# Kernel optimization log

Hardware: AMD Instinct MI355X
Metric: run time of the kernel (lower is better)

Reference implementation:

```python
import jax, jax.numpy as jnp
import numpy as np
import math

K_DIM = 1024
HEADS = 16

def setup_inputs() -> dict:
    key = jax.random.key(0)
    ks = jax.random.split(key, 6)
    b, N, k = 4, 2048, K_DIM
    sc = 1.0 / math.sqrt(k)
    return {
        "x": jax.random.normal(ks[0], (b, N, k), dtype=jnp.float32),
        "Wk": jax.random.normal(ks[1], (k, k), dtype=jnp.float32) * sc,
        "Wq": jax.random.normal(ks[2], (k, k), dtype=jnp.float32) * sc,
        "Wv": jax.random.normal(ks[3], (k, k), dtype=jnp.float32) * sc,
        "Wu": jax.random.normal(ks[4], (k, k), dtype=jnp.float32) * sc,
        "bu": jax.random.normal(ks[5], (k,), dtype=jnp.float32) * 0.01,
    }

def reference(x, Wk, Wq, Wv, Wu, bu):
    b, N, k = x.shape
    h = HEADS
    s = k // h
    # torch Linear: y = x @ W^T
    Q = (x @ Wq.T).reshape(b, N, h, s).transpose(0, 2, 1, 3)  # [b,h,N,s]
    Kh = (x @ Wk.T).reshape(b, N, h, s).transpose(0, 2, 1, 3)
    V = (x @ Wv.T).reshape(b, N, h, s).transpose(0, 2, 1, 3)
    scores = jnp.einsum('bhid,bhjd->bhij', Q, Kh) / math.sqrt(s)  # [b,h,N,N]
    attn = jax.nn.softmax(scores, axis=-1)
    out = jnp.einsum('bhij,bhjd->bhid', attn, V)  # [b,h,N,s]
    out = out.transpose(0, 2, 1, 3).reshape(b, N, k)
    return out @ Wu.T + bu
```

## Files before the change

### kernel.cpp

```cpp
#include <hip/hip_runtime.h>

typedef __bf16 bf16;
typedef __bf16 bf16x4 __attribute__((ext_vector_type(4)));
typedef __bf16 bf16x8 __attribute__((ext_vector_type(8)));
typedef float  f32x4  __attribute__((ext_vector_type(4)));

#define MFMA16(a, b, c) __builtin_amdgcn_mfma_f32_16x16x32_bf16((a), (b), (c), 0, 0, 0)

__device__ __forceinline__ void async_copy16(const void* g, void* l) {
  __builtin_amdgcn_global_load_lds(
      (const __attribute__((address_space(1))) unsigned int*)g,
      (__attribute__((address_space(3))) unsigned int*)l, 16, 0, 0);
}

struct CvtArgs {
  const float* src[5];
  bf16* dst[5];
  int blk_start[6];
};
__global__ void k_cvt_all(CvtArgs a) {
  int b = blockIdx.x;
  int seg = 0;
#pragma unroll
  for (int s = 1; s < 5; ++s) seg += (b >= a.blk_start[s]);
  int i = (b - a.blk_start[seg]) * 2048 + threadIdx.x * 8;
  float4 v0 = *(const float4*)(a.src[seg] + i);
  float4 v1 = *(const float4*)(a.src[seg] + i + 4);
  bf16x8 o = { (bf16)v0.x, (bf16)v0.y, (bf16)v0.z, (bf16)v0.w,
               (bf16)v1.x, (bf16)v1.y, (bf16)v1.z, (bf16)v1.w };
  *(bf16x8*)(a.dst[seg] + i) = o;
}

template <int OUTF32>
__device__ __forceinline__ void gemm128_body(
    const bf16* __restrict__ A, const bf16* __restrict__ B, void* __restrict__ Cp,
    const float* __restrict__ bias, int m0, int n0, int N, int K) {
  __shared__ alignas(16) bf16 As[2][128 * 32];
  __shared__ alignas(16) bf16 Bs[2][128 * 32];
  const int tid = threadIdx.x;
  const int lane = tid & 63;
  const int w = tid >> 6;
  const int quad = lane >> 4;
  const int l16 = lane & 15;
  const int wr = (w >> 1) * 64;
  const int wc = (w & 1) * 64;

  const int srow = tid >> 2;
  const int skk = (tid & 3) * 8;
  const bf16* Ag = A + (long)(m0 + srow) * K + skk;
  const bf16* Bg = B + (long)(n0 + srow) * K + skk;
  const long half = 64L * K;
  bf16* AsW0 = As[0] + w * 512;
  bf16* BsW0 = Bs[0] + w * 512;
  bf16* AsW1 = As[1] + w * 512;
  bf16* BsW1 = Bs[1] + w * 512;

  f32x4 acc[4][4];
#pragma unroll
  for (int i = 0; i < 4; ++i)
#pragma unroll
    for (int j = 0; j < 4; ++j) acc[i][j] = (f32x4){0.f, 0.f, 0.f, 0.f};

  for (int k0 = 0; k0 < K; k0 += 64) {
    async_copy16(Ag + k0, AsW0);
    async_copy16(Ag + half + k0, AsW0 + 2048);
    async_copy16(Bg + k0, BsW0);
    async_copy16(Bg + half + k0, BsW0 + 2048);
    async_copy16(Ag + k0 + 32, AsW1);
    async_copy16(Ag + half + k0 + 32, AsW1 + 2048);
    async_copy16(Bg + k0 + 32, BsW1);
    async_copy16(Bg + half + k0 + 32, BsW1 + 2048);
    __syncthreads();
#pragma unroll
    for (int p = 0; p < 2; ++p) {
      const bf16* AsP = As[p];
      const bf16* BsP = Bs[p];
      bf16x8 af[4], bfr[4];
#pragma unroll
      for (int i = 0; i < 4; ++i)
        af[i] = *(const bf16x8*)&AsP[(wr + i * 16 + l16) * 32 + quad * 8];
#pragma unroll
      for (int j = 0; j < 4; ++j)
        bfr[j] = *(const bf16x8*)&BsP[(wc + j * 16 + l16) * 32 + quad * 8];
#pragma unroll
      for (int i = 0; i < 4; ++i)
#pragma unroll
        for (int j = 0; j < 4; ++j) acc[i][j] = MFMA16(af[i], bfr[j], acc[i][j]);
    }
    __syncthreads();
  }

#pragma unroll
  for (int i = 0; i < 4; ++i)
#pragma unroll
    for (int j = 0; j < 4; ++j)
#pragma unroll
      for (int r = 0; r < 4; ++r) {
        long row = m0 + wr + i * 16 + quad * 4 + r;
        int col = n0 + wc + j * 16 + l16;
        if (OUTF32)
          ((float*)Cp)[row * N + col] = acc[i][j][r] + bias[col];
        else
          ((bf16*)Cp)[row * N + col] = (bf16)acc[i][j][r];
      }
}

__global__ __launch_bounds__(256, 4) void k_gemm_qkv(
    const bf16* __restrict__ xb, const bf16* __restrict__ Wqk, bf16* __restrict__ QKb,
    const bf16* __restrict__ Wvb, bf16* __restrict__ VtG) {
  int bid = blockIdx.x;
  const bf16 *A, *B;
  bf16* C;
  int m0, n0, N;
  if (bid < 1024) {
    A = xb; B = Wqk; C = QKb;
    m0 = (bid & 63) * 128; n0 = (bid >> 6) * 128; N = 2048;
  } else {
    int id = bid - 1024;
    A = Wvb; B = xb; C = VtG;
    m0 = (id >> 6) * 128; n0 = (id & 63) * 128; N = 8192;
  }
  gemm128_body<0>(A, B, C, nullptr, m0, n0, N, 1024);
}

__global__ __launch_bounds__(256, 4) void k_gemm_out(
    const bf16* __restrict__ Ab, const bf16* __restrict__ Wub, float* __restrict__ out,
    const float* __restrict__ bu) {
  gemm128_body<1>(Ab, Wub, out, bu, blockIdx.x * 128, blockIdx.y * 128, 1024, 1024);
}

__global__ __launch_bounds__(256, 2) void k_attn(
    const bf16* __restrict__ Q, const bf16* __restrict__ Kb,
    const bf16* __restrict__ Vt, bf16* __restrict__ O) {
  __shared__ alignas(16) bf16 Ps[256][72];
  __shared__ alignas(16) bf16 Ks[64][72];
  __shared__ alignas(16) bf16 Vs[64][72];

  const int tid = threadIdx.x;
  const int lane = tid & 63;
  const int w = tid >> 6;
  const int quad = lane >> 4;
  const int l16 = lane & 15;
  const int bh = blockIdx.x;
  const int qt = blockIdx.y;
  const int bb = bh >> 4;
  const int h = bh & 15;
  const int hoff = h * 64;
  const long rowQ0 = (long)bb * 2048 + qt * 256;
  const long kv0 = (long)bb * 2048;

  {
    const bf16* p = Q + (rowQ0 + tid) * 2048 + hoff;
#pragma unroll
    for (int u = 0; u < 8; ++u) {
      bf16x8 v = *(const bf16x8*)(p + u * 8);
      bf16x8 o;
#pragma unroll
      for (int j = 0; j < 8; ++j) o[j] = (bf16)((float)v[j] * 0.125f);
      *(bf16x8*)&Ps[tid][u * 8] = o;
    }
  }
  bf16x8 bq[4][2];
#pragma unroll
  for (int g = 0; g < 4; ++g)
#pragma unroll
    for (int ss = 0; ss < 2; ++ss)
      bq[g][ss] = *(const bf16x8*)&Ps[w * 64 + g * 16 + l16][ss * 32 + quad * 8];

  f32x4 accO[4][4];
  float lp[4] = {0.f, 0.f, 0.f, 0.f};
#pragma unroll
  for (int g = 0; g < 4; ++g)
#pragma unroll
    for (int t = 0; t < 4; ++t) accO[g][t] = (f32x4){0.f, 0.f, 0.f, 0.f};

  const int srow = tid >> 2;
  const int scol = (tid & 3) * 8;
  const int c0p = ((scol & 8) << 1) | ((scol & 16) >> 2);
  const bf16* kp = Kb + (kv0 + srow) * 2048 + hoff + scol;
  const bf16* vp = Vt + (long)(hoff + srow) * 8192 + kv0 + scol;

  bf16x8 kr0 = *(const bf16x8*)kp;
  bf16x8 kr1 = *(const bf16x8*)(kp + 32);
  bf16x8 vr0 = *(const bf16x8*)vp;
  bf16x8 vr1 = *(const bf16x8*)(vp + 32);

  for (int kt = 0; kt < 32; ++kt) {
    __syncthreads();
    *(bf16x8*)&Ks[srow][scol] = kr0;
    *(bf16x8*)&Ks[srow][scol + 32] = kr1;
    {
      bf16x4 lo0 = {vr0[0], vr0[1], vr0[2], vr0[3]};
      bf16x4 hi0 = {vr0[4], vr0[5], vr0[6], vr0[7]};
      bf16x4 lo1 = {vr1[0], vr1[1], vr1[2], vr1[3]};
      bf16x4 hi1 = {vr1[4], vr1[5], vr1[6], vr1[7]};
      *(bf16x4*)&Vs[srow][c0p] = lo0;
      *(bf16x4*)&Vs[srow][c0p + 8] = hi0;
      *(bf16x4*)&Vs[srow][c0p + 32] = lo1;
      *(bf16x4*)&Vs[srow][c0p + 40] = hi1;
    }
    __syncthreads();
    if (kt < 31) {
      const bf16* kp2 = kp + (long)(kt + 1) * 64 * 2048;
      const bf16* vp2 = vp + (kt + 1) * 64;
      kr0 = *(const bf16x8*)kp2;
      kr1 = *(const bf16x8*)(kp2 + 32);
      vr0 = *(const bf16x8*)vp2;
      vr1 = *(const bf16x8*)(vp2 + 32);
    }

    bf16x8 ak[4][2], bv[2][4];
#pragma unroll
    for (int mt = 0; mt < 4; ++mt) {
      ak[mt][0] = *(const bf16x8*)&Ks[mt * 16 + l16][quad * 8];
      ak[mt][1] = *(const bf16x8*)&Ks[mt * 16 + l16][32 + quad * 8];
    }
#pragma unroll
    for (int ss = 0; ss < 2; ++ss)
#pragma unroll
      for (int t = 0; t < 4; ++t)
        bv[ss][t] = *(const bf16x8*)&Vs[t * 16 + l16][ss * 32 + quad * 8];

#pragma unroll
    for (int g = 0; g < 4; ++g) {
      f32x4 st[4];
#pragma unroll
      for (int mt = 0; mt < 4; ++mt) {
        st[mt] = (f32x4){0.f, 0.f, 0.f, 0.f};
        st[mt] = MFMA16(ak[mt][0], bq[g][0], st[mt]);
        st[mt] = MFMA16(ak[mt][1], bq[g][1], st[mt]);
      }
      bf16x8 apf[2];
#pragma unroll
      for (int mt = 0; mt < 4; ++mt) {
#pragma unroll
        for (int r = 0; r < 4; ++r) {
          float pv = __expf(st[mt][r]);
          lp[g] += pv;
          apf[mt >> 1][(mt & 1) * 4 + r] = (bf16)pv;
        }
      }
#pragma unroll
      for (int ss = 0; ss < 2; ++ss)
#pragma unroll
        for (int t = 0; t < 4; ++t)
          accO[g][t] = MFMA16(apf[ss], bv[ss][t], accO[g][t]);
    }
  }

#pragma unroll
  for (int g = 0; g < 4; ++g) {
    float l = lp[g];
    l += __shfl_xor(l, 16);
    l += __shfl_xor(l, 32);
    float linv = 1.f / l;
#pragma unroll
    for (int r = 0; r < 4; ++r) {
      float inv = __shfl(linv, (lane & 48) | (quad * 4 + r));
      long row = rowQ0 + w * 64 + g * 16 + quad * 4 + r;
#pragma unroll
      for (int t = 0; t < 4; ++t)
        O[row * 1024 + hoff + t * 16 + l16] = (bf16)(accO[g][t][r] * inv);
    }
  }
}

extern "C" void kernel_launch(void* const* d_in, const int* in_sizes, int n_in,
                              void* d_out, int out_size, void* d_ws, size_t ws_size,
                              hipStream_t stream) {
  const float* x  = (const float*)d_in[0];
  const float* Wk = (const float*)d_in[1];
  const float* Wq = (const float*)d_in[2];
  const float* Wv = (const float*)d_in[3];
  const float* Wu = (const float*)d_in[4];
  const float* bu = (const float*)d_in[5];
  float* out = (float*)d_out;

  const int XE = 4 * 2048 * 1024;
  const int WE = 1024 * 1024;

  bf16* p = (bf16*)d_ws;
  bf16* xb   = p; p += XE;
  bf16* Wqkb = p; p += 2 * WE;
  bf16* Wvb  = p; p += WE;
  bf16* Wub  = p; p += WE;
  bf16* QKb  = p; p += 2 * XE;
  bf16* VtG  = p; p += XE;
  bf16* Ab   = p; p += XE;

  CvtArgs ca;
  ca.src[0] = x;  ca.dst[0] = xb;
  ca.src[1] = Wq; ca.dst[1] = Wqkb;
  ca.src[2] = Wk; ca.dst[2] = Wqkb + WE;
  ca.src[3] = Wv; ca.dst[3] = Wvb;
  ca.src[4] = Wu; ca.dst[4] = Wub;
  ca.blk_start[0] = 0;
  ca.blk_start[1] = XE / 2048;
  ca.blk_start[2] = ca.blk_start[1] + WE / 2048;
  ca.blk_start[3] = ca.blk_start[2] + WE / 2048;
  ca.blk_start[4] = ca.blk_start[3] + WE / 2048;
  ca.blk_start[5] = ca.blk_start[4] + WE / 2048;
  k_cvt_all<<<ca.blk_start[5], 256, 0, stream>>>(ca);

  k_gemm_qkv<<<1536, 256, 0, stream>>>(xb, Wqkb, QKb, Wvb, VtG);

  k_attn<<<dim3(64, 8), 256, 0, stream>>>(QKb, QKb + 1024, VtG, Ab);

  k_gemm_out<<<dim3(64, 8), 256, 0, stream>>>(Ab, Wub, out, bu);
}
```

Measured before the change: 252.8 us.

## Double-buffer K/V tiles via async global-to-LDS copies with XOR swizzle

The attention kernel now loads K and V tiles straight into LDS with global_load_lds async copies, double-buffered so the next tile streams in while the current one is computed. This removes the register staging, the per-thread LDS stores and one barrier per iteration. The LDS layout gains an XOR swizzle to avoid bank conflicts, and Q is loaded directly into registers without an LDS round trip. The softmax row sum is now computed with an extra MFMA against a ones vector instead of scalar adds and shuffles, which adds matrix work but drops the VALU accumulation. The single barrier per iteration must also cover async-copy completion and reuse of the buffer being overwritten, which is a correctness risk.

```diff
diff --git a/kernel.cpp b/kernel.cpp
--- a/kernel.cpp
+++ b/kernel.cpp
@@ -132,15 +132,16 @@
 __global__ __launch_bounds__(256, 2) void k_attn(
     const bf16* __restrict__ Q, const bf16* __restrict__ Kb,
     const bf16* __restrict__ Vt, bf16* __restrict__ O) {
-  __shared__ alignas(16) bf16 Ps[256][72];
-  __shared__ alignas(16) bf16 Ks[64][72];
-  __shared__ alignas(16) bf16 Vs[64][72];
+  __shared__ alignas(16) bf16 Ks[2][64 * 64];
+  __shared__ alignas(16) bf16 Vs[2][64 * 64];
 
   const int tid = threadIdx.x;
   const int lane = tid & 63;
   const int w = tid >> 6;
   const int quad = lane >> 4;
   const int l16 = lane & 15;
+  const int hsw = l16 & 7;
+  const int h2 = hsw << 1;
   const int bh = blockIdx.x;
   const int qt = blockIdx.y;
   const int bb = bh >> 4;
@@ -149,77 +150,76 @@
   const long rowQ0 = (long)bb * 2048 + qt * 256;
   const long kv0 = (long)bb * 2048;
 
-  {
-    const bf16* p = Q + (rowQ0 + tid) * 2048 + hoff;
-#pragma unroll
-    for (int u = 0; u < 8; ++u) {
-      bf16x8 v = *(const bf16x8*)(p + u * 8);
+  bf16x8 bq[4][2];
+#pragma unroll
+  for (int g = 0; g < 4; ++g)
+#pragma unroll
+    for (int ss = 0; ss < 2; ++ss) {
+      const bf16* p = Q + (rowQ0 + w * 64 + g * 16 + l16) * 2048 + hoff + ss * 32 + quad * 8;
+      bf16x8 v = *(const bf16x8*)p;
       bf16x8 o;
 #pragma unroll
       for (int j = 0; j < 8; ++j) o[j] = (bf16)((float)v[j] * 0.125f);
-      *(bf16x8*)&Ps[tid][u * 8] = o;
-    }
+      bq[g][ss] = o;
+    }
+
+  f32x4 accO[4][4];
+  f32x4 accS[4];
+#pragma unroll
+  for (int g = 0; g < 4; ++g) {
+    accS[g] = (f32x4){0.f, 0.f, 0.f, 0.f};
+#pragma unroll
+    for (int t = 0; t < 4; ++t) accO[g][t] = (f32x4){0.f, 0.f, 0.f, 0.f};
   }
-  bf16x8 bq[4][2];
-#pragma unroll
-  for (int g = 0; g < 4; ++g)
-#pragma unroll
-    for (int ss = 0; ss < 2; ++ss)
-      bq[g][ss] = *(const bf16x8*)&Ps[w * 64 + g * 16 + l16][ss * 32 + quad * 8];
-
-  f32x4 accO[4][4];
-  float lp[4] = {0.f, 0.f, 0.f, 0.f};
-#pragma unroll
-  for (int g = 0; g < 4; ++g)
-#pragma unroll
-    for (int t = 0; t < 4; ++t) accO[g][t] = (f32x4){0.f, 0.f, 0.f, 0.f};
-
-  const int srow = tid >> 2;
-  const int scol = (tid & 3) * 8;
-  const int c0p = ((scol & 8) << 1) | ((scol & 16) >> 2);
-  const bf16* kp = Kb + (kv0 + srow) * 2048 + hoff + scol;
-  const bf16* vp = Vt + (long)(hoff + srow) * 8192 + kv0 + scol;
-
-  bf16x8 kr0 = *(const bf16x8*)kp;
-  bf16x8 kr1 = *(const bf16x8*)(kp + 32);
-  bf16x8 vr0 = *(const bf16x8*)vp;
-  bf16x8 vr1 = *(const bf16x8*)(vp + 32);
+
+  const int rr = tid >> 3;
+  const int cc8 = ((tid & 7) ^ (rr & 7)) * 8;
+  const bf16* ksrc = Kb + (kv0 + rr) * 2048 + hoff + cc8;
+  const bf16* vsrc = Vt + (long)(hoff + rr) * 8192 + kv0 + cc8;
+  const int dstOff = w * 512;
+
+  async_copy16(ksrc, Ks[0] + dstOff);
+  async_copy16(ksrc + 32 * 2048, Ks[0] + 2048 + dstOff);
+  async_copy16(vsrc, Vs[0] + dstOff);
+  async_copy16(vsrc + 32 * 8192, Vs[0] + 2048 + dstOff);
+  ksrc += 64 * 2048;
+  vsrc += 64;
+
+  const bf16 onev = (bf16)1.0f;
+  const bf16x8 ones8 = {onev, onev, onev, onev, onev, onev, onev, onev};
 
   for (int kt = 0; kt < 32; ++kt) {
     __syncthreads();
-    *(bf16x8*)&Ks[srow][scol] = kr0;
-    *(bf16x8*)&Ks[srow][scol + 32] = kr1;
-    {
-      bf16x4 lo0 = {vr0[0], vr0[1], vr0[2], vr0[3]};
-      bf16x4 hi0 = {vr0[4], vr0[5], vr0[6], vr0[7]};
-      bf16x4 lo1 = {vr1[0], vr1[1], vr1[2], vr1[3]};
-      bf16x4 hi1 = {vr1[4], vr1[5], vr1[6], vr1[7]};
-      *(bf16x4*)&Vs[srow][c0p] = lo0;
-      *(bf16x4*)&Vs[srow][c0p + 8] = hi0;
-      *(bf16x4*)&Vs[srow][c0p + 32] = lo1;
-      *(bf16x4*)&Vs[srow][c0p + 40] = hi1;
-    }
-    __syncthreads();
     if (kt < 31) {
-      const bf16* kp2 = kp + (long)(kt + 1) * 64 * 2048;
-      const bf16* vp2 = vp + (kt + 1) * 64;
-      kr0 = *(const bf16x8*)kp2;
-      kr1 = *(const bf16x8*)(kp2 + 32);
-      vr0 = *(const bf16x8*)vp2;
-      vr1 = *(const bf16x8*)(vp2 + 32);
-    }
-
-    bf16x8 ak[4][2], bv[2][4];
+      bf16* kb = Ks[(kt + 1) & 1];
+      bf16* vb = Vs[(kt + 1) & 1];
+      async_copy16(ksrc, kb + dstOff);
+      async_copy16(ksrc + 32 * 2048, kb + 2048 + dstOff);
+      async_copy16(vsrc, vb + dstOff);
+      async_copy16(vsrc + 32 * 8192, vb + 2048 + dstOff);
+      ksrc += 64 * 2048;
+      vsrc += 64;
+    }
+    const bf16* kbuf = Ks[kt & 1];
+    const bf16* vbuf = Vs[kt & 1];
+
+    bf16x8 ak[4][2];
 #pragma unroll
     for (int mt = 0; mt < 4; ++mt) {
-      ak[mt][0] = *(const bf16x8*)&Ks[mt * 16 + l16][quad * 8];
-      ak[mt][1] = *(const bf16x8*)&Ks[mt * 16 + l16][32 + quad * 8];
-    }
+      const int rb = (mt * 16 + l16) * 64;
+      ak[mt][0] = *(const bf16x8*)&kbuf[rb + ((quad ^ hsw) * 8)];
+      ak[mt][1] = *(const bf16x8*)&kbuf[rb + (((4 + quad) ^ hsw) * 8)];
+    }
+    bf16x8 bv[2][4];
 #pragma unroll
     for (int ss = 0; ss < 2; ++ss)
 #pragma unroll
-      for (int t = 0; t < 4; ++t)
-        bv[ss][t] = *(const bf16x8*)&Vs[t * 16 + l16][ss * 32 + quad * 8];
+      for (int t = 0; t < 4; ++t) {
+        const int rb = (t * 16 + l16) * 64;
+        bf16x4 lo = *(const bf16x4*)&vbuf[rb + (((ss * 8 + quad) ^ h2) * 4)];
+        bf16x4 hi = *(const bf16x4*)&vbuf[rb + (((ss * 8 + 4 + quad) ^ h2) * 4)];
+        bv[ss][t] = __builtin_shufflevector(lo, hi, 0, 1, 2, 3, 4, 5, 6, 7);
+      }
 
 #pragma unroll
     for (int g = 0; g < 4; ++g) {
@@ -236,33 +236,29 @@
 #pragma unroll
         for (int r = 0; r < 4; ++r) {
           float pv = __expf(st[mt][r]);
-          lp[g] += pv;
           apf[mt >> 1][(mt & 1) * 4 + r] = (bf16)pv;
         }
       }
 #pragma unroll
-      for (int ss = 0; ss < 2; ++ss)
+      for (int ss = 0; ss < 2; ++ss) {
 #pragma unroll
         for (int t = 0; t < 4; ++t)
           accO[g][t] = MFMA16(apf[ss], bv[ss][t], accO[g][t]);
+        accS[g] = MFMA16(apf[ss], ones8, accS[g]);
+      }
     }
   }
 
 #pragma unroll
-  for (int g = 0; g < 4; ++g) {
-    float l = lp[g];
-    l += __shfl_xor(l, 16);
-    l += __shfl_xor(l, 32);
-    float linv = 1.f / l;
+  for (int g = 0; g < 4; ++g)
 #pragma unroll
     for (int r = 0; r < 4; ++r) {
-      float inv = __shfl(linv, (lane & 48) | (quad * 4 + r));
+      float inv = 1.f / accS[g][r];
       long row = rowQ0 + w * 64 + g * 16 + quad * 4 + r;
 #pragma unroll
       for (int t = 0; t < 4; ++t)
         O[row * 1024 + hoff + t * 16 + l16] = (bf16)(accO[g][t][r] * inv);
     }
-  }
 }
 
 extern "C" void kernel_launch(void* const* d_in, const int* in_sizes, int n_in,
```

Result: no change. 253.1 us (+0.2%).
